# Kernel optimization log

Measured on AMD Instinct MI355X. Metric: run time of the kernel, lower is better.

## Reference

```python
import jax, jax.numpy as jnp
import numpy as np

N = 100000   # nodes
E = 625000   # edges
D = 128      # feature / embedding dim
C = 40       # num classes
BN_EPS = 1e-5
L2_EPS = 1e-12


def setup_inputs() -> dict:
    key = jax.random.key(0)
    ks = jax.random.split(key, 8)
    s = 1.0 / np.sqrt(D)
    return {
        "x": jax.random.normal(ks[0], (N, D), dtype=jnp.float32),
        "edge_index": jax.random.randint(ks[1], (2, E), 0, N, dtype=jnp.int64),
        "W1": jax.random.normal(ks[2], (D, D), dtype=jnp.float32) * s,
        "b1": jnp.zeros((D,), jnp.float32),
        "W2": jax.random.normal(ks[3], (D, D), dtype=jnp.float32) * s,
        "b2": jnp.zeros((D,), jnp.float32),
        "W3": jax.random.normal(ks[4], (D, D), dtype=jnp.float32) * s,
        "b3": jnp.zeros((D,), jnp.float32),
        "g1": jnp.ones((D,), jnp.float32), "be1": jnp.zeros((D,), jnp.float32),
        "g2": jnp.ones((D,), jnp.float32), "be2": jnp.zeros((D,), jnp.float32),
        "g3": jnp.ones((D,), jnp.float32), "be3": jnp.zeros((D,), jnp.float32),
        "Wout": jax.random.normal(ks[5], (D, C), dtype=jnp.float32) * s,
        "bout": jnp.zeros((C,), jnp.float32),
    }


def _gcn_norm(edge_index, n):
    # PyG GCNConv default: add self loops, symmetric normalization
    loop = jnp.arange(n)
    src = jnp.concatenate([edge_index[0], loop])
    dst = jnp.concatenate([edge_index[1], loop])
    deg = jax.ops.segment_sum(jnp.ones_like(src, dtype=jnp.float32), dst, num_segments=n)
    dinv = jnp.where(deg > 0, jax.lax.rsqrt(deg), 0.0)
    norm = dinv[src] * dinv[dst]  # [E+N]
    return src, dst, norm


def _gcn_conv(x, W, b, src, dst, norm, n):
    h = x @ W                                # [N, D]
    msg = h[src] * norm[:, None]             # gather, [E+N, D]
    out = jax.ops.segment_sum(msg, dst, num_segments=n)  # scatter-add
    return out + b


def _bn(x, g, b):
    mu = jnp.mean(x, axis=0)
    var = jnp.var(x, axis=0)
    return (x - mu) * jax.lax.rsqrt(var + BN_EPS) * g + b


def _l2norm(x):
    n = jnp.sqrt(jnp.sum(x * x, axis=1, keepdims=True))
    return x / jnp.maximum(n, L2_EPS)


def reference(x, edge_index, W1, b1, W2, b2, W3, b3,
              g1, be1, g2, be2, g3, be3, Wout, bout):
    n = x.shape[0]
    src, dst, norm = _gcn_norm(edge_index, n)

    h = jax.nn.relu(_bn(_gcn_conv(x, W1, b1, src, dst, norm, n), g1, be1))
    h = _l2norm(h)
    r = h
    h = jax.nn.relu(_bn(_gcn_conv(h, W2, b2, src, dst, norm, n), g2, be2))
    h = _l2norm(h + r)
    r = h
    h = jax.nn.relu(_bn(_gcn_conv(h, W3, b3, src, dst, norm, n), g3, be3))
    h = _l2norm(h + r)

    return h @ Wout + bout  # node classification logits [N, C]
```

## Files before the change

kernel.cpp:

```cpp
#include <hip/hip_runtime.h>
#include <math.h>

#define DD 128
#define COUT 40
#define BN_EPS 1e-5f
#define L2_EPS 1e-12f
#define NREP 64

typedef __attribute__((ext_vector_type(8))) short bf16x8;
typedef __attribute__((ext_vector_type(4))) float f32x4;

static __device__ inline unsigned short f2bf(float f) {
    unsigned int x = __float_as_uint(f);
    unsigned int r = (x + 0x7FFFu + ((x >> 16) & 1u)) >> 16;
    return (unsigned short)r;
}
static __device__ inline float bf2f(unsigned short u) {
    return __uint_as_float(((unsigned int)u) << 16);
}


__global__ void k_hist(const int* __restrict__ ei, int E, int* __restrict__ deg,
                       int* __restrict__ pord) {
    int i = blockIdx.x * blockDim.x + threadIdx.x;
    if (i < E) pord[i] = atomicAdd(&deg[ei[E + i]], 1);
}

__global__ void k_scan_a(const int* __restrict__ deg, int* __restrict__ row_ptr,
                         int* __restrict__ bsum, float* __restrict__ dinv, int n) {
    __shared__ int s[256];
    int t = threadIdx.x;
    int idx = blockIdx.x * 256 + t;
    int v = (idx < n) ? deg[idx] + 1 : 0;
    if (idx < n) dinv[idx] = rsqrtf((float)v);
    s[t] = v; __syncthreads();
    for (int off = 1; off < 256; off <<= 1) {
        int x = (t >= off) ? s[t - off] : 0;
        __syncthreads(); s[t] += x; __syncthreads();
    }
    if (idx <= n) row_ptr[idx] = s[t] - v;
    if (t == 255) bsum[blockIdx.x] = s[255];
}

__global__ void k_scan_b(const int* __restrict__ bsum, int* __restrict__ boff, int nb) {
    __shared__ int s[512];
    int t = threadIdx.x;
    int v = (t < nb) ? bsum[t] : 0;
    s[t] = v; __syncthreads();
    for (int off = 1; off < 512; off <<= 1) {
        int x = (t >= off) ? s[t - off] : 0;
        __syncthreads(); s[t] += x; __syncthreads();
    }
    if (t < nb) boff[t] = s[t] - v;
}

__global__ void k_scan_c(int* __restrict__ row_ptr, const int* __restrict__ boff, int n1) {
    int idx = blockIdx.x * blockDim.x + threadIdx.x;
    if (idx < n1) row_ptr[idx] += boff[idx >> 8];
}

__global__ void k_fill(const int* __restrict__ ei, const int* __restrict__ pord,
                       int E, int n, const int* __restrict__ row_ptr,
                       const float* __restrict__ dinv, int2* __restrict__ epair) {
    int i = blockIdx.x * blockDim.x + threadIdx.x;
    int total = E + n;
    if (i >= total) return;
    int u, pos;
    if (i < E) {
        u = ei[i];
        int v = ei[E + i];
        pos = row_ptr[v] + pord[i];
    } else {
        u = i - E;
        pos = row_ptr[u + 1] - 1;
    }
    int2 pr; pr.x = u; pr.y = __float_as_int(dinv[u]);
    epair[pos] = pr;
}

__global__ void k_wrepack_all(const float* __restrict__ W1, const float* __restrict__ W2,
                              const float* __restrict__ W3, const float* __restrict__ Wout,
                              unsigned short* __restrict__ wb,
                              unsigned short* __restrict__ wob,
                              float* __restrict__ stats) {
    int b = blockIdx.x;
    if (b < 24) {
        int wi = b >> 3;
        const float* W = (wi == 0) ? W1 : (wi == 1) ? W2 : W3;
        unsigned short* out = wb + wi * 16384;
        int idx = (b & 7) * 256 + threadIdx.x;
        int kc = idx >> 9;
        int cc = (idx >> 6) & 7;
        int lane = idx & 63;
        int n = cc * 16 + (lane & 15);
        int kb = kc * 32 + (lane >> 4) * 8;
        unsigned short tmp[8];
#pragma unroll
        for (int j = 0; j < 8; j++) tmp[j] = f2bf(W[(size_t)(kb + j) * DD + n]);
        *(uint4*)&out[(size_t)idx * 8] = *(const uint4*)tmp;
    } else if (b < 27) {
        int idx = (b - 24) * 256 + threadIdx.x;
        int kc = idx / 192;
        int rem = idx % 192;
        int cc = rem >> 6;
        int lane = rem & 63;
        int n = cc * 16 + (lane & 15);
        int kb = kc * 32 + (lane >> 4) * 8;
        unsigned short tmp[8];
#pragma unroll
        for (int j = 0; j < 8; j++)
            tmp[j] = (n < COUT) ? f2bf(Wout[(size_t)(kb + j) * COUT + n]) : 0;
        *(uint4*)&wob[(size_t)idx * 8] = *(const uint4*)tmp;
    } else {
        float4 z = make_float4(0.f, 0.f, 0.f, 0.f);
        int idx = (b - 27) * 256 + threadIdx.x;
        for (int i = idx; i < 3 * NREP * 64; i += 8 * 256)
            ((float4*)stats)[i] = z;
    }
}


__global__ __launch_bounds__(256) void k_gemm0(const float* __restrict__ A,
                                               const unsigned short* __restrict__ Wb,
                                               unsigned short* __restrict__ C, int nrows) {
    __shared__ __align__(16) unsigned short Ws[16384];
    const int tid = threadIdx.x;
    for (int i = tid; i < 2048; i += 256)
        ((uint4*)Ws)[i] = ((const uint4*)Wb)[i];
    __syncthreads();

    const int wv = tid >> 6;
    const int lane = tid & 63;
    const int R0 = blockIdx.x * 64 + wv * 16;
    if (R0 >= nrows) return;
    const int m = lane & 15, q = lane >> 4;
    int rr = R0 + m; if (rr >= nrows) rr = nrows - 1;
    const float* Ar = A + (size_t)rr * DD + q * 8;

    bf16x8 af[4];
#pragma unroll
    for (int kc = 0; kc < 4; kc++) {
        float4 lo = *(const float4*)(Ar + kc * 32);
        float4 hi = *(const float4*)(Ar + kc * 32 + 4);
        unsigned short t[8];
        t[0] = f2bf(lo.x); t[1] = f2bf(lo.y); t[2] = f2bf(lo.z); t[3] = f2bf(lo.w);
        t[4] = f2bf(hi.x); t[5] = f2bf(hi.y); t[6] = f2bf(hi.z); t[7] = f2bf(hi.w);
        af[kc] = *(const bf16x8*)t;
    }

    f32x4 acc[8];
#pragma unroll
    for (int cc = 0; cc < 8; cc++) acc[cc] = (f32x4){0.f, 0.f, 0.f, 0.f};
#pragma unroll
    for (int kc = 0; kc < 4; kc++)
#pragma unroll
        for (int cc = 0; cc < 8; cc++) {
            bf16x8 b = *(const bf16x8*)&Ws[(size_t)((kc * 8 + cc) * 64 + lane) * 8];
            acc[cc] = __builtin_amdgcn_mfma_f32_16x16x32_bf16(af[kc], b, acc[cc], 0, 0, 0);
        }

#pragma unroll
    for (int cc = 0; cc < 8; cc++)
#pragma unroll
        for (int i = 0; i < 4; i++) {
            int r = R0 + q * 4 + i;
            if (r < nrows) C[(size_t)r * DD + cc * 16 + m] = f2bf(acc[cc][i]);
        }
}

__global__ __launch_bounds__(256) void k_aggs(const unsigned short* __restrict__ lin,
                                              const int* __restrict__ row_ptr,
                                              const int2* __restrict__ epair,
                                              const float* __restrict__ dinv,
                                              const float* __restrict__ bias,
                                              unsigned short* __restrict__ outb,
                                              float* __restrict__ stats, int n) {
    const int tid = threadIdx.x;
    const int wv = tid >> 6;
    const int lane = tid & 63;
    const int half = lane >> 5;
    const int li = lane & 31;
    const int slot = li >> 4;
    const int ci = (li & 15) * 8;

    const int v = blockIdx.x * 8 + wv * 2 + half;
    const bool valid = v < n;

    float acc[8];
#pragma unroll
    for (int k = 0; k < 8; k++) acc[k] = 0.f;

    if (valid) {
        const int s0 = row_ptr[v];
        const int e0 = row_ptr[v + 1];
        const float dv = dinv[v];
        for (int j = s0; j < e0; j += 4) {
            int i0 = j + slot;
            int i1 = j + 2 + slot;
            bool b0 = i0 < e0;
            bool b1 = i1 < e0;
            int2 p0, p1;
            if (b0) p0 = epair[i0];
            if (b1) p1 = epair[i1];
            if (b0) {
                float w = dv * __int_as_float(p0.y);
                uint4 t = *(const uint4*)&lin[(size_t)p0.x * DD + ci];
                acc[0] += w * __uint_as_float(t.x << 16);
                acc[1] += w * __uint_as_float(t.x & 0xFFFF0000u);
                acc[2] += w * __uint_as_float(t.y << 16);
                acc[3] += w * __uint_as_float(t.y & 0xFFFF0000u);
                acc[4] += w * __uint_as_float(t.z << 16);
                acc[5] += w * __uint_as_float(t.z & 0xFFFF0000u);
                acc[6] += w * __uint_as_float(t.w << 16);
                acc[7] += w * __uint_as_float(t.w & 0xFFFF0000u);
            }
            if (b1) {
                float w = dv * __int_as_float(p1.y);
                uint4 t = *(const uint4*)&lin[(size_t)p1.x * DD + ci];
                acc[0] += w * __uint_as_float(t.x << 16);
                acc[1] += w * __uint_as_float(t.x & 0xFFFF0000u);
                acc[2] += w * __uint_as_float(t.y << 16);
                acc[3] += w * __uint_as_float(t.y & 0xFFFF0000u);
                acc[4] += w * __uint_as_float(t.z << 16);
                acc[5] += w * __uint_as_float(t.z & 0xFFFF0000u);
                acc[6] += w * __uint_as_float(t.w << 16);
                acc[7] += w * __uint_as_float(t.w & 0xFFFF0000u);
            }
        }
    }
#pragma unroll
    for (int k = 0; k < 8; k++) acc[k] += __shfl_xor(acc[k], 16, 64);

    __shared__ float sh[8][128];
    __shared__ float qh[8][128];
    const int prow = wv * 2 + half;
    if (slot == 0) {
        if (valid) {
            float4 bb0 = *(const float4*)&bias[ci];
            float4 bb1 = *(const float4*)&bias[ci + 4];
            float bs[8] = {bb0.x, bb0.y, bb0.z, bb0.w, bb1.x, bb1.y, bb1.z, bb1.w};
            unsigned short t[8];
#pragma unroll
            for (int k = 0; k < 8; k++) {
                float a = acc[k] + bs[k];
                t[k] = f2bf(a);
                sh[prow][ci + k] = a;
                qh[prow][ci + k] = a * a;
            }
            *(uint4*)&outb[(size_t)v * DD + ci] = *(const uint4*)t;
        } else {
#pragma unroll
            for (int k = 0; k < 8; k++) { sh[prow][ci + k] = 0.f; qh[prow][ci + k] = 0.f; }
        }
    }
    __syncthreads();
    if (tid < 128) {
        float a = 0.f, b = 0.f;
#pragma unroll
        for (int g = 0; g < 8; g++) { a += sh[g][tid]; b += qh[g][tid]; }
        float* st = stats + (size_t)(blockIdx.x & (NREP - 1)) * 256;
        atomicAdd(&st[tid], a);
        atomicAdd(&st[128 + tid], b);
    }
}

template <bool HAS_RES>
__global__ __launch_bounds__(256) void k_fused(const unsigned short* __restrict__ aggX,
                                               const float* __restrict__ stats,
                                               const float* __restrict__ g,
                                               const float* __restrict__ be, float inv_n,
                                               const unsigned short* __restrict__ resb,
                                               const unsigned short* __restrict__ Wb,
                                               unsigned short* __restrict__ hbf_out,
                                               unsigned short* __restrict__ linb_out,
                                               int nrows) {
    __shared__ __align__(16) unsigned short Ws[16384];
    __shared__ float ssl[256];
    const int tid = threadIdx.x;
    for (int i = tid; i < 2048; i += 256)
        ((uint4*)Ws)[i] = ((const uint4*)Wb)[i];
    if (tid < 128) {
        float sa = 0.f, sb = 0.f;
        for (int r = 0; r < NREP; r++) {
            sa += stats[r * 256 + tid];
            sb += stats[r * 256 + 128 + tid];
        }
        float mu = sa * inv_n;
        float var = sb * inv_n - mu * mu;
        float sc = g[tid] * rsqrtf(var + BN_EPS);
        ssl[tid] = sc;
        ssl[128 + tid] = be[tid] - mu * sc;
    }
    __syncthreads();

    const int wv = tid >> 6;
    const int lane = tid & 63;
    const int R0 = blockIdx.x * 64 + wv * 16;
    if (R0 >= nrows) return;
    const int m = lane & 15, q = lane >> 4;
    int rr = R0 + m; if (rr >= nrows) rr = nrows - 1;
    const unsigned short* Ar = aggX + (size_t)rr * DD + q * 8;
    const unsigned short* Rr = HAS_RES ? resb + (size_t)rr * DD + q * 8 : nullptr;

    float y[4][8];
    float sq = 0.f;
#pragma unroll
    for (int kc = 0; kc < 4; kc++) {
        ushort4 lo = *(const ushort4*)(Ar + kc * 32);
        ushort4 hi = *(const ushort4*)(Ar + kc * 32 + 4);
        unsigned short av[8] = {lo.x, lo.y, lo.z, lo.w, hi.x, hi.y, hi.z, hi.w};
        int c0 = kc * 32 + q * 8;
        float4 sc0 = *(const float4*)&ssl[c0];
        float4 sc1 = *(const float4*)&ssl[c0 + 4];
        float4 sh0 = *(const float4*)&ssl[128 + c0];
        float4 sh1 = *(const float4*)&ssl[128 + c0 + 4];
        float scv[8] = {sc0.x, sc0.y, sc0.z, sc0.w, sc1.x, sc1.y, sc1.z, sc1.w};
        float shv[8] = {sh0.x, sh0.y, sh0.z, sh0.w, sh1.x, sh1.y, sh1.z, sh1.w};
        if (HAS_RES) {
            ushort4 rl = *(const ushort4*)(Rr + kc * 32);
            ushort4 rh = *(const ushort4*)(Rr + kc * 32 + 4);
            unsigned short rv[8] = {rl.x, rl.y, rl.z, rl.w, rh.x, rh.y, rh.z, rh.w};
#pragma unroll
            for (int j = 0; j < 8; j++) {
                float yy = fmaxf(bf2f(av[j]) * scv[j] + shv[j], 0.f) + bf2f(rv[j]);
                y[kc][j] = yy; sq += yy * yy;
            }
        } else {
#pragma unroll
            for (int j = 0; j < 8; j++) {
                float yy = fmaxf(bf2f(av[j]) * scv[j] + shv[j], 0.f);
                y[kc][j] = yy; sq += yy * yy;
            }
        }
    }
    sq += __shfl_xor(sq, 16, 64);
    sq += __shfl_xor(sq, 32, 64);
    float inv = 1.f / fmaxf(sqrtf(sq), L2_EPS);

    bf16x8 af[4];
#pragma unroll
    for (int kc = 0; kc < 4; kc++) {
        unsigned short t[8];
#pragma unroll
        for (int j = 0; j < 8; j++) t[j] = f2bf(y[kc][j] * inv);
        af[kc] = *(const bf16x8*)t;
        *(bf16x8*)&hbf_out[(size_t)rr * DD + q * 8 + kc * 32] = af[kc];
    }

    f32x4 acc[8];
#pragma unroll
    for (int cc = 0; cc < 8; cc++) acc[cc] = (f32x4){0.f, 0.f, 0.f, 0.f};
#pragma unroll
    for (int kc = 0; kc < 4; kc++)
#pragma unroll
        for (int cc = 0; cc < 8; cc++) {
            bf16x8 b = *(const bf16x8*)&Ws[(size_t)((kc * 8 + cc) * 64 + lane) * 8];
            acc[cc] = __builtin_amdgcn_mfma_f32_16x16x32_bf16(af[kc], b, acc[cc], 0, 0, 0);
        }

#pragma unroll
    for (int cc = 0; cc < 8; cc++)
#pragma unroll
        for (int i = 0; i < 4; i++) {
            int r = R0 + q * 4 + i;
            if (r < nrows) linb_out[(size_t)r * DD + cc * 16 + m] = f2bf(acc[cc][i]);
        }
}

__global__ __launch_bounds__(256) void k_outfused(const unsigned short* __restrict__ aggX,
                                                  const float* __restrict__ stats,
                                                  const float* __restrict__ g,
                                                  const float* __restrict__ be, float inv_n,
                                                  const unsigned short* __restrict__ resb,
                                                  const unsigned short* __restrict__ wob,
                                                  const float* __restrict__ bout,
                                                  float* __restrict__ C, int nrows) {
    __shared__ __align__(16) unsigned short Ws[6144];
    __shared__ float ssl[256];
    const int tid = threadIdx.x;
    for (int i = tid; i < 768; i += 256)
        ((uint4*)Ws)[i] = ((const uint4*)wob)[i];
    if (tid < 128) {
        float sa = 0.f, sb = 0.f;
        for (int r = 0; r < NREP; r++) {
            sa += stats[r * 256 + tid];
            sb += stats[r * 256 + 128 + tid];
        }
        float mu = sa * inv_n;
        float var = sb * inv_n - mu * mu;
        float sc = g[tid] * rsqrtf(var + BN_EPS);
        ssl[tid] = sc;
        ssl[128 + tid] = be[tid] - mu * sc;
    }
    __syncthreads();

    const int wv = tid >> 6;
    const int lane = tid & 63;
    const int R0 = blockIdx.x * 64 + wv * 16;
    if (R0 >= nrows) return;
    const int m = lane & 15, q = lane >> 4;
    int rr = R0 + m; if (rr >= nrows) rr = nrows - 1;
    const unsigned short* Ar = aggX + (size_t)rr * DD + q * 8;
    const unsigned short* Rr = resb + (size_t)rr * DD + q * 8;

    float y[4][8];
    float sq = 0.f;
#pragma unroll
    for (int kc = 0; kc < 4; kc++) {
        ushort4 lo = *(const ushort4*)(Ar + kc * 32);
        ushort4 hi = *(const ushort4*)(Ar + kc * 32 + 4);
        ushort4 rl = *(const ushort4*)(Rr + kc * 32);
        ushort4 rh = *(const ushort4*)(Rr + kc * 32 + 4);
        unsigned short av[8] = {lo.x, lo.y, lo.z, lo.w, hi.x, hi.y, hi.z, hi.w};
        unsigned short rv[8] = {rl.x, rl.y, rl.z, rl.w, rh.x, rh.y, rh.z, rh.w};
        int c0 = kc * 32 + q * 8;
        float4 sc0 = *(const float4*)&ssl[c0];
        float4 sc1 = *(const float4*)&ssl[c0 + 4];
        float4 sh0 = *(const float4*)&ssl[128 + c0];
        float4 sh1 = *(const float4*)&ssl[128 + c0 + 4];
        float scv[8] = {sc0.x, sc0.y, sc0.z, sc0.w, sc1.x, sc1.y, sc1.z, sc1.w};
        float shv[8] = {sh0.x, sh0.y, sh0.z, sh0.w, sh1.x, sh1.y, sh1.z, sh1.w};
#pragma unroll
        for (int j = 0; j < 8; j++) {
            float yy = fmaxf(bf2f(av[j]) * scv[j] + shv[j], 0.f) + bf2f(rv[j]);
            y[kc][j] = yy; sq += yy * yy;
        }
    }
    sq += __shfl_xor(sq, 16, 64);
    sq += __shfl_xor(sq, 32, 64);
    float inv = 1.f / fmaxf(sqrtf(sq), L2_EPS);

    bf16x8 af[4];
#pragma unroll
    for (int kc = 0; kc < 4; kc++) {
        unsigned short t[8];
#pragma unroll
        for (int j = 0; j < 8; j++) t[j] = f2bf(y[kc][j] * inv);
        af[kc] = *(const bf16x8*)t;
    }

    f32x4 acc[3];
#pragma unroll
    for (int cc = 0; cc < 3; cc++) acc[cc] = (f32x4){0.f, 0.f, 0.f, 0.f};
#pragma unroll
    for (int kc = 0; kc < 4; kc++)
#pragma unroll
        for (int cc = 0; cc < 3; cc++) {
            bf16x8 b = *(const bf16x8*)&Ws[(size_t)((kc * 3 + cc) * 64 + lane) * 8];
            acc[cc] = __builtin_amdgcn_mfma_f32_16x16x32_bf16(af[kc], b, acc[cc], 0, 0, 0);
        }

#pragma unroll
    for (int cc = 0; cc < 3; cc++) {
        int col = cc * 16 + m;
        if (col < COUT) {
            float bb = bout[col];
#pragma unroll
            for (int i = 0; i < 4; i++) {
                int r = R0 + q * 4 + i;
                if (r < nrows) C[(size_t)r * COUT + col] = acc[cc][i] + bb;
            }
        }
    }
}


extern "C" void kernel_launch(void* const* d_in, const int* in_sizes, int n_in,
                              void* d_out, int out_size, void* d_ws, size_t ws_size,
                              hipStream_t stream) {
    const float* x    = (const float*)d_in[0];
    const int*   ei   = (const int*)d_in[1];
    const float* W1   = (const float*)d_in[2];
    const float* b1   = (const float*)d_in[3];
    const float* W2   = (const float*)d_in[4];
    const float* b2   = (const float*)d_in[5];
    const float* W3   = (const float*)d_in[6];
    const float* b3   = (const float*)d_in[7];
    const float* g1   = (const float*)d_in[8];
    const float* be1  = (const float*)d_in[9];
    const float* g2   = (const float*)d_in[10];
    const float* be2  = (const float*)d_in[11];
    const float* g3   = (const float*)d_in[12];
    const float* be3  = (const float*)d_in[13];
    const float* Wout = (const float*)d_in[14];
    const float* bout = (const float*)d_in[15];
    float* out = (float*)d_out;

    const int N = in_sizes[0] / DD;
    const int E = in_sizes[1] / 2;
    const int NNZ = E + N;
    const int SSTRIDE = NREP * 256;

    char* w = (char*)d_ws;
    unsigned short* linb = (unsigned short*)w; w += (size_t)N * DD * sizeof(unsigned short);
    unsigned short* aggA = (unsigned short*)w; w += (size_t)N * DD * sizeof(unsigned short);
    unsigned short* aggB = (unsigned short*)w; w += (size_t)N * DD * sizeof(unsigned short);
    unsigned short* hbf1 = (unsigned short*)w; w += (size_t)N * DD * sizeof(unsigned short);
    unsigned short* hbf2 = (unsigned short*)w; w += (size_t)N * DD * sizeof(unsigned short);
    unsigned short* wb   = (unsigned short*)w; w += 3 * 16384 * sizeof(unsigned short);
    unsigned short* wob  = (unsigned short*)w; w += 6144 * sizeof(unsigned short);
    int2* epair  = (int2*)w;                   w += (size_t)NNZ * sizeof(int2);
    int* pord    = (int*)w;                    w += (size_t)E * sizeof(int);
    int* deg     = (int*)w;                    w += (size_t)N * sizeof(int);
    int* row_ptr = (int*)w;                    w += (size_t)(N + 1) * sizeof(int);
    float* dinv  = (float*)w;                  w += (size_t)N * sizeof(float);
    int* bsum    = (int*)w;                    w += 512 * sizeof(int);
    int* boff    = (int*)w;                    w += 512 * sizeof(int);
    float* stats = (float*)w;                  w += 3 * (size_t)SSTRIDE * sizeof(float);

    const int NB = (N + 1 + 255) / 256;

    hipMemsetAsync(deg, 0, (size_t)N * sizeof(int), stream);
    k_wrepack_all<<<35, 256, 0, stream>>>(W1, W2, W3, Wout, wb, wob, stats);
    k_hist<<<(E + 255) / 256, 256, 0, stream>>>(ei, E, deg, pord);
    k_scan_a<<<NB, 256, 0, stream>>>(deg, row_ptr, bsum, dinv, N);
    k_scan_b<<<1, 512, 0, stream>>>(bsum, boff, NB);
    k_scan_c<<<(N + 1 + 255) / 256, 256, 0, stream>>>(row_ptr, boff, N + 1);
    k_fill<<<(NNZ + 255) / 256, 256, 0, stream>>>(ei, pord, E, N, row_ptr, dinv, epair);

    int gemmGrid = (N + 63) / 64;
    int aggGrid = (N + 7) / 8;
    float inv_n = 1.0f / (float)N;

    k_gemm0<<<gemmGrid, 256, 0, stream>>>(x, wb, linb, N);
    k_aggs<<<aggGrid, 256, 0, stream>>>(linb, row_ptr, epair, dinv, b1, aggA, stats, N);
    k_fused<false><<<gemmGrid, 256, 0, stream>>>(aggA, stats, g1, be1, inv_n,
                                                 nullptr, wb + 16384, hbf1, linb, N);
    k_aggs<<<aggGrid, 256, 0, stream>>>(linb, row_ptr, epair, dinv, b2, aggB,
                                        stats + SSTRIDE, N);
    k_fused<true><<<gemmGrid, 256, 0, stream>>>(aggB, stats + SSTRIDE, g2, be2, inv_n,
                                                hbf1, wb + 32768, hbf2, linb, N);
    k_aggs<<<aggGrid, 256, 0, stream>>>(linb, row_ptr, epair, dinv, b3, aggA,
                                        stats + 2 * SSTRIDE, N);
    k_outfused<<<gemmGrid, 256, 0, stream>>>(aggA, stats + 2 * SSTRIDE, g3, be3, inv_n,
                                             hbf2, wob, bout, out, N);
}
```

Baseline: 391.5 us.

## Fold source degree scaling into GEMM epilogue and unroll gather loop

Pre-scales each transformed row by its own inverse-sqrt degree in the GEMM epilogue and applies the destination degree once after aggregation. This lets the edge list carry only source indices (int instead of int2) and removes the per-edge multiply. The aggregation loop now handles 8 edges per iteration with all row loads issued before accumulation, giving more memory-level parallelism. The cost is slightly different rounding, since scaling happens before the bf16 store, and higher register use in the gather kernel.

```diff
diff --git a/kernel.cpp b/kernel.cpp
--- a/kernel.cpp
+++ b/kernel.cpp
@@ -61,7 +61,7 @@
 
 __global__ void k_fill(const int* __restrict__ ei, const int* __restrict__ pord,
                        int E, int n, const int* __restrict__ row_ptr,
-                       const float* __restrict__ dinv, int2* __restrict__ epair) {
+                       int* __restrict__ perm) {
     int i = blockIdx.x * blockDim.x + threadIdx.x;
     int total = E + n;
     if (i >= total) return;
@@ -74,8 +74,7 @@
         u = i - E;
         pos = row_ptr[u + 1] - 1;
     }
-    int2 pr; pr.x = u; pr.y = __float_as_int(dinv[u]);
-    epair[pos] = pr;
+    perm[pos] = u;
 }
 
 __global__ void k_wrepack_all(const float* __restrict__ W1, const float* __restrict__ W2,
@@ -122,6 +121,7 @@
 
 __global__ __launch_bounds__(256) void k_gemm0(const float* __restrict__ A,
                                                const unsigned short* __restrict__ Wb,
+                                               const float* __restrict__ dinv,
                                                unsigned short* __restrict__ C, int nrows) {
     __shared__ __align__(16) unsigned short Ws[16384];
     const int tid = threadIdx.x;
@@ -159,18 +159,24 @@
             acc[cc] = __builtin_amdgcn_mfma_f32_16x16x32_bf16(af[kc], b, acc[cc], 0, 0, 0);
         }
 
+    float dr[4];
+#pragma unroll
+    for (int i = 0; i < 4; i++) {
+        int r = R0 + q * 4 + i;
+        dr[i] = (r < nrows) ? dinv[r] : 0.f;
+    }
 #pragma unroll
     for (int cc = 0; cc < 8; cc++)
 #pragma unroll
         for (int i = 0; i < 4; i++) {
             int r = R0 + q * 4 + i;
-            if (r < nrows) C[(size_t)r * DD + cc * 16 + m] = f2bf(acc[cc][i]);
+            if (r < nrows) C[(size_t)r * DD + cc * 16 + m] = f2bf(acc[cc][i] * dr[i]);
         }
 }
 
 __global__ __launch_bounds__(256) void k_aggs(const unsigned short* __restrict__ lin,
                                               const int* __restrict__ row_ptr,
-                                              const int2* __restrict__ epair,
+                                              const int* __restrict__ perm,
                                               const float* __restrict__ dinv,
                                               const float* __restrict__ bias,
                                               unsigned short* __restrict__ outb,
@@ -189,42 +195,67 @@
     float acc[8];
 #pragma unroll
     for (int k = 0; k < 8; k++) acc[k] = 0.f;
+    float dv = 0.f;
 
     if (valid) {
         const int s0 = row_ptr[v];
         const int e0 = row_ptr[v + 1];
-        const float dv = dinv[v];
-        for (int j = s0; j < e0; j += 4) {
+        dv = dinv[v];
+        for (int j = s0; j < e0; j += 8) {
             int i0 = j + slot;
             int i1 = j + 2 + slot;
-            bool b0 = i0 < e0;
-            bool b1 = i1 < e0;
-            int2 p0, p1;
-            if (b0) p0 = epair[i0];
-            if (b1) p1 = epair[i1];
+            int i2 = j + 4 + slot;
+            int i3 = j + 6 + slot;
+            bool b0 = i0 < e0, b1 = i1 < e0, b2 = i2 < e0, b3 = i3 < e0;
+            int u0, u1, u2, u3;
+            if (b0) u0 = perm[i0];
+            if (b1) u1 = perm[i1];
+            if (b2) u2 = perm[i2];
+            if (b3) u3 = perm[i3];
+            uint4 t0, t1, t2, t3;
+            if (b0) t0 = *(const uint4*)&lin[(size_t)u0 * DD + ci];
+            if (b1) t1 = *(const uint4*)&lin[(size_t)u1 * DD + ci];
+            if (b2) t2 = *(const uint4*)&lin[(size_t)u2 * DD + ci];
+            if (b3) t3 = *(const uint4*)&lin[(size_t)u3 * DD + ci];
             if (b0) {
-                float w = dv * __int_as_float(p0.y);
-                uint4 t = *(const uint4*)&lin[(size_t)p0.x * DD + ci];
-                acc[0] += w * __uint_as_float(t.x << 16);
-                acc[1] += w * __uint_as_float(t.x & 0xFFFF0000u);
-                acc[2] += w * __uint_as_float(t.y << 16);
-                acc[3] += w * __uint_as_float(t.y & 0xFFFF0000u);
-                acc[4] += w * __uint_as_float(t.z << 16);
-                acc[5] += w * __uint_as_float(t.z & 0xFFFF0000u);
-                acc[6] += w * __uint_as_float(t.w << 16);
-                acc[7] += w * __uint_as_float(t.w & 0xFFFF0000u);
+                acc[0] += __uint_as_float(t0.x << 16);
+                acc[1] += __uint_as_float(t0.x & 0xFFFF0000u);
+                acc[2] += __uint_as_float(t0.y << 16);
+                acc[3] += __uint_as_float(t0.y & 0xFFFF0000u);
+                acc[4] += __uint_as_float(t0.z << 16);
+                acc[5] += __uint_as_float(t0.z & 0xFFFF0000u);
+                acc[6] += __uint_as_float(t0.w << 16);
+                acc[7] += __uint_as_float(t0.w & 0xFFFF0000u);
             }
             if (b1) {
-                float w = dv * __int_as_float(p1.y);
-                uint4 t = *(const uint4*)&lin[(size_t)p1.x * DD + ci];
-                acc[0] += w * __uint_as_float(t.x << 16);
-                acc[1] += w * __uint_as_float(t.x & 0xFFFF0000u);
-                acc[2] += w * __uint_as_float(t.y << 16);
-                acc[3] += w * __uint_as_float(t.y & 0xFFFF0000u);
-                acc[4] += w * __uint_as_float(t.z << 16);
-                acc[5] += w * __uint_as_float(t.z & 0xFFFF0000u);
-                acc[6] += w * __uint_as_float(t.w << 16);
-                acc[7] += w * __uint_as_float(t.w & 0xFFFF0000u);
+                acc[0] += __uint_as_float(t1.x << 16);
+                acc[1] += __uint_as_float(t1.x & 0xFFFF0000u);
+                acc[2] += __uint_as_float(t1.y << 16);
+                acc[3] += __uint_as_float(t1.y & 0xFFFF0000u);
+                acc[4] += __uint_as_float(t1.z << 16);
+                acc[5] += __uint_as_float(t1.z & 0xFFFF0000u);
+                acc[6] += __uint_as_float(t1.w << 16);
+                acc[7] += __uint_as_float(t1.w & 0xFFFF0000u);
+            }
+            if (b2) {
+                acc[0] += __uint_as_float(t2.x << 16);
+                acc[1] += __uint_as_float(t2.x & 0xFFFF0000u);
+                acc[2] += __uint_as_float(t2.y << 16);
+                acc[3] += __uint_as_float(t2.y & 0xFFFF0000u);
+                acc[4] += __uint_as_float(t2.z << 16);
+                acc[5] += __uint_as_float(t2.z & 0xFFFF0000u);
+                acc[6] += __uint_as_float(t2.w << 16);
+                acc[7] += __uint_as_float(t2.w & 0xFFFF0000u);
+            }
+            if (b3) {
+                acc[0] += __uint_as_float(t3.x << 16);
+                acc[1] += __uint_as_float(t3.x & 0xFFFF0000u);
+                acc[2] += __uint_as_float(t3.y << 16);
+                acc[3] += __uint_as_float(t3.y & 0xFFFF0000u);
+                acc[4] += __uint_as_float(t3.z << 16);
+                acc[5] += __uint_as_float(t3.z & 0xFFFF0000u);
+                acc[6] += __uint_as_float(t3.w << 16);
+                acc[7] += __uint_as_float(t3.w & 0xFFFF0000u);
             }
         }
     }
@@ -242,7 +273,7 @@
             unsigned short t[8];
 #pragma unroll
             for (int k = 0; k < 8; k++) {
-                float a = acc[k] + bs[k];
+                float a = acc[k] * dv + bs[k];
                 t[k] = f2bf(a);
                 sh[prow][ci + k] = a;
                 qh[prow][ci + k] = a * a;
@@ -271,6 +302,7 @@
                                                const float* __restrict__ be, float inv_n,
                                                const unsigned short* __restrict__ resb,
                                                const unsigned short* __restrict__ Wb,
+                                               const float* __restrict__ dinv,
                                                unsigned short* __restrict__ hbf_out,
                                                unsigned short* __restrict__ linb_out,
                                                int nrows) {
@@ -358,12 +390,18 @@
             acc[cc] = __builtin_amdgcn_mfma_f32_16x16x32_bf16(af[kc], b, acc[cc], 0, 0, 0);
         }
 
+    float dr[4];
+#pragma unroll
+    for (int i = 0; i < 4; i++) {
+        int r = R0 + q * 4 + i;
+        dr[i] = (r < nrows) ? dinv[r] : 0.f;
+    }
 #pragma unroll
     for (int cc = 0; cc < 8; cc++)
 #pragma unroll
         for (int i = 0; i < 4; i++) {
             int r = R0 + q * 4 + i;
-            if (r < nrows) linb_out[(size_t)r * DD + cc * 16 + m] = f2bf(acc[cc][i]);
+            if (r < nrows) linb_out[(size_t)r * DD + cc * 16 + m] = f2bf(acc[cc][i] * dr[i]);
         }
 }
 
@@ -499,7 +537,7 @@
     unsigned short* hbf2 = (unsigned short*)w; w += (size_t)N * DD * sizeof(unsigned short);
     unsigned short* wb   = (unsigned short*)w; w += 3 * 16384 * sizeof(unsigned short);
     unsigned short* wob  = (unsigned short*)w; w += 6144 * sizeof(unsigned short);
-    int2* epair  = (int2*)w;                   w += (size_t)NNZ * sizeof(int2);
+    int* perm    = (int*)w;                    w += (size_t)NNZ * sizeof(int);
     int* pord    = (int*)w;                    w += (size_t)E * sizeof(int);
     int* deg     = (int*)w;                    w += (size_t)N * sizeof(int);
     int* row_ptr = (int*)w;                    w += (size_t)(N + 1) * sizeof(int);
@@ -516,21 +554,21 @@
     k_scan_a<<<NB, 256, 0, stream>>>(deg, row_ptr, bsum, dinv, N);
     k_scan_b<<<1, 512, 0, stream>>>(bsum, boff, NB);
     k_scan_c<<<(N + 1 + 255) / 256, 256, 0, stream>>>(row_ptr, boff, N + 1);
-    k_fill<<<(NNZ + 255) / 256, 256, 0, stream>>>(ei, pord, E, N, row_ptr, dinv, epair);
+    k_fill<<<(NNZ + 255) / 256, 256, 0, stream>>>(ei, pord, E, N, row_ptr, perm);
 
     int gemmGrid = (N + 63) / 64;
     int aggGrid = (N + 7) / 8;
     float inv_n = 1.0f / (float)N;
 
-    k_gemm0<<<gemmGrid, 256, 0, stream>>>(x, wb, linb, N);
-    k_aggs<<<aggGrid, 256, 0, stream>>>(linb, row_ptr, epair, dinv, b1, aggA, stats, N);
+    k_gemm0<<<gemmGrid, 256, 0, stream>>>(x, wb, dinv, linb, N);
+    k_aggs<<<aggGrid, 256, 0, stream>>>(linb, row_ptr, perm, dinv, b1, aggA, stats, N);
     k_fused<false><<<gemmGrid, 256, 0, stream>>>(aggA, stats, g1, be1, inv_n,
-                                                 nullptr, wb + 16384, hbf1, linb, N);
-    k_aggs<<<aggGrid, 256, 0, stream>>>(linb, row_ptr, epair, dinv, b2, aggB,
+                                                 nullptr, wb + 16384, dinv, hbf1, linb, N);
+    k_aggs<<<aggGrid, 256, 0, stream>>>(linb, row_ptr, perm, dinv, b2, aggB,
                                         stats + SSTRIDE, N);
     k_fused<true><<<gemmGrid, 256, 0, stream>>>(aggB, stats + SSTRIDE, g2, be2, inv_n,
-                                                hbf1, wb + 32768, hbf2, linb, N);
-    k_aggs<<<aggGrid, 256, 0, stream>>>(linb, row_ptr, epair, dinv, b3, aggA,
+                                                hbf1, wb + 32768, dinv, hbf2, linb, N);
+    k_aggs<<<aggGrid, 256, 0, stream>>>(linb, row_ptr, perm, dinv, b3, aggA,
                                         stats + 2 * SSTRIDE, N);
     k_outfused<<<gemmGrid, 256, 0, stream>>>(aggA, stats + 2 * SSTRIDE, g3, be3, inv_n,
                                              hbf2, wob, bout, out, N);
```

Measured after the change: 404.5 us. 3.3% more time.
